# Performance work log

Hardware: AMD Instinct MI355X
Metric: run time of the kernel (lower is better)

Reference implementation:

```python
import jax, jax.numpy as jnp
import numpy as np

# pywt db8 reconstruction low-pass filter (rec_lo); other filters derived per pywt conventions
_REC_LO = np.array([
    0.05441584224308161, 0.3128715909144659, 0.6756307362980128,
    0.5853546836548691, -0.015829105256023893, -0.2840155429624281,
    0.00047248457399797254, 0.128747426620186, -0.01736930100202211,
    -0.04408825393106472, 0.013981027917015516, 0.008746094047015655,
    -0.00487035299301066, -0.0003917403729959771, 0.0006754494059985568,
    -0.00011747678400228192], dtype=np.float64)
_F = 16
_REC_HI = np.array([(-1.0) ** k * _REC_LO[_F - 1 - k] for k in range(_F)])  # qmf
_DEC_LO = _REC_LO[::-1].copy()
_DEC_HI = _REC_HI[::-1].copy()
# lax.conv does cross-correlation; np.convolve flips the filter, so pre-flip here
_DEC_K = np.ascontiguousarray(np.stack([_DEC_LO[::-1], _DEC_HI[::-1]])[:, None, :])  # [2,1,F]
_REC_K = np.ascontiguousarray(np.stack([_REC_LO[::-1], _REC_HI[::-1]])[None, :, :])  # [1,2,F]
_THRESHOLD_FACTOR = 1.0


def _dwt_last(x):
    # single-level DWT along last axis, pywt 'symmetric' boundary mode
    shp = x.shape
    xf = x.reshape(-1, 1, shp[-1])
    xe = jnp.pad(xf, ((0, 0), (0, 0), (_F - 1, _F - 1)), mode='symmetric')[:, :, 1:]
    y = jax.lax.conv_general_dilated(xe, jnp.asarray(_DEC_K, x.dtype), (2,), 'VALID',
                                     dimension_numbers=('NCW', 'OIW', 'NCW'))  # [M,2,n]
    n = y.shape[-1]  # n = floor((N + F - 1) / 2)
    return y[:, 0].reshape(shp[:-1] + (n,)), y[:, 1].reshape(shp[:-1] + (n,))


def _idwt_last(ca, cd, out_len):
    # single-level inverse DWT along last axis; out_len = 2*n - F + 2
    shp = ca.shape
    n = shp[-1]
    m = int(np.prod(shp[:-1]))
    u = jnp.zeros((m, 2, 2 * n), ca.dtype)
    u = u.at[:, 0, ::2].set(ca.reshape(m, n)).at[:, 1, ::2].set(cd.reshape(m, n))
    ue = jnp.pad(u, ((0, 0), (0, 0), (_F - 1, _F - 1)))
    y = jax.lax.conv_general_dilated(ue, jnp.asarray(_REC_K, ca.dtype), (1,), 'VALID',
                                     dimension_numbers=('NCW', 'OIW', 'NCW'))[:, 0]
    return y[:, _F - 2:_F - 2 + out_len].reshape(shp[:-1] + (out_len,))


def _forward(x):
    B, H, W, C = x.shape
    M = B * C
    xm = jnp.transpose(x, (0, 3, 1, 2)).reshape(M, H, W)
    # level-1 wavedec2: rows (W axis) then columns (H axis)
    lo, hi = _dwt_last(xm)                               # [M,H,nW]
    ll, lh = _dwt_last(jnp.swapaxes(lo, -1, -2))         # [M,nW,nH]
    hl, hh = _dwt_last(jnp.swapaxes(hi, -1, -2))         # [M,nW,nH]
    # universal threshold from median abs of all detail subbands, per sample/channel
    det = jnp.concatenate([lh.reshape(M, -1), hl.reshape(M, -1), hh.reshape(M, -1)], axis=-1)
    sigma = jnp.median(jnp.abs(det), axis=-1) / 0.6745
    t = (sigma * jnp.sqrt(2.0 * jnp.log(float(H * W))) * _THRESHOLD_FACTOR)[:, None, None]
    soft = lambda c: jnp.sign(c) * jnp.maximum(jnp.abs(c) - t, 0.0)
    lh, hl, hh = soft(lh), soft(hl), soft(hh)
    # waverec2: inverse along H then along W
    nH = ll.shape[-1]
    Hr = 2 * nH - _F + 2
    rl = jnp.swapaxes(_idwt_last(ll, lh, Hr), -1, -2)    # [M,Hr,nW]
    rh = jnp.swapaxes(_idwt_last(hl, hh, Hr), -1, -2)    # [M,Hr,nW]
    nW = rl.shape[-1]
    y = _idwt_last(rl, rh, 2 * nW - _F + 2)              # [M,Hr,Wr]
    y = y[:, :H, :W].reshape(B, C, H, W)
    return jnp.transpose(y, (0, 2, 3, 1)).astype(x.dtype)


def setup_inputs() -> dict:
    key = jax.random.key(0)
    x = jax.random.normal(key, (32, 512, 512, 3), dtype=jnp.float32)
    return {"x": x}


def reference(x):
    return _forward(x)
```

## Files before the change

kernel.cpp:

```cpp
#include <hip/hip_runtime.h>
#include <math.h>

#define B_   32
#define H_   512
#define W_   512
#define C_   3
#define M_   96
#define NW_  263
#define NH_  263
#define DETPER 69169
#define DETTOT 207507
#define DETSTRIDE 207508
#define NVEC 51876
#define KRANK  103753u

__device__ __constant__ float RLO[16] = {
    0.05441584224308161f,  0.3128715909144659f,   0.6756307362980128f,
    0.5853546836548691f,  -0.015829105256023893f, -0.2840155429624281f,
    0.00047248457399797254f, 0.128747426620186f,  -0.01736930100202211f,
   -0.04408825393106472f,  0.013981027917015516f,  0.008746094047015655f,
   -0.00487035299301066f, -0.0003917403729959771f, 0.0006754494059985568f,
   -0.00011747678400228192f};
__device__ __constant__ float RHI[16] = {
   -0.00011747678400228192f, -0.0006754494059985568f, -0.0003917403729959771f,
    0.00487035299301066f,     0.008746094047015655f,  -0.013981027917015516f,
   -0.04408825393106472f,     0.01736930100202211f,    0.128747426620186f,
   -0.00047248457399797254f, -0.2840155429624281f,     0.015829105256023893f,
    0.5853546836548691f,     -0.6756307362980128f,     0.3128715909144659f,
   -0.05441584224308161f};

__device__ __forceinline__ int refl(int q, int N) {
    if (q < 0)  return -q - 1;
    if (q >= N) return 2 * N - 1 - q;
    return q;
}

__device__ __forceinline__ float softthr(float v, float thr) {
    float a = fabsf(v) - thr;
    return a > 0.f ? copysignf(a, v) : 0.f;
}

__global__ __launch_bounds__(256) void k_zero(unsigned* __restrict__ p, int n) {
    int i = blockIdx.x * 256 + threadIdx.x;
    if (i < n) p[i] = 0u;
}

__global__ __launch_bounds__(256) void k_fwd(const float* __restrict__ x,
                                             float* __restrict__ ll,
                                             float* __restrict__ det) {
    __shared__ float sX[46 * 144];
    __shared__ float sLO[46 * 64], sHI[46 * 64];
    const int m   = blockIdx.x;
    const int jw0 = blockIdx.y * 64;
    const int jh0 = blockIdx.z * 16;
    const int b = m / 3, c = m - 3 * (m / 3);
    const int tid = threadIdx.x;
    const int prow0 = 2 * jh0 - 14, pcol0 = 2 * jw0 - 14;
    for (int l = tid; l < 46 * 142; l += 256) {
        int rr = l / 142, cl = l - rr * 142;
        int h = refl(prow0 + rr, H_);
        int w = refl(pcol0 + cl, W_);
        sX[rr * 144 + cl] = x[((size_t)(b * H_ + h) * W_ + w) * C_ + c];
    }
    __syncthreads();
    for (int l = tid; l < 46 * 64; l += 256) {
        int rr = l >> 6, j = l & 63;
        const float* px = &sX[rr * 144 + 2 * j];
        float al = 0.f, ah = 0.f;
#pragma unroll
        for (int k = 0; k < 16; ++k) {
            al = fmaf(px[k], RLO[k], al);
            ah = fmaf(px[k], RHI[k], ah);
        }
        sLO[l] = al;
        sHI[l] = ah;
    }
    __syncthreads();
    const int tx = tid & 63, ty = tid >> 6;
    const int jw = jw0 + tx;
    if (jw >= NW_) return;
    float* llp = ll + (size_t)m * DETPER;
    float* dp  = det + (size_t)m * DETSTRIDE;
#pragma unroll
    for (int i = 0; i < 4; ++i) {
        int dy = ty + 4 * i;
        int jh = jh0 + dy;
        if (jh >= NH_) continue;
        int rbase = 2 * dy;
        float a0 = 0.f, a1 = 0.f, a2 = 0.f, a3 = 0.f;
#pragma unroll
        for (int k = 0; k < 16; ++k) {
            float vl = sLO[(rbase + k) * 64 + tx];
            float vh = sHI[(rbase + k) * 64 + tx];
            a0 = fmaf(vl, RLO[k], a0);
            a1 = fmaf(vl, RHI[k], a1);
            a2 = fmaf(vh, RLO[k], a2);
            a3 = fmaf(vh, RHI[k], a3);
        }
        size_t o = (size_t)jh * NW_ + jw;
        llp[o] = a0;
        dp[o] = a1;
        dp[DETPER + o] = a2;
        dp[2 * DETPER + o] = a3;
    }
}

__global__ __launch_bounds__(256) void k_hist1(const float* __restrict__ det,
                                               unsigned* __restrict__ hist) {
    __shared__ unsigned h[2048];
    const int tid = threadIdx.x, m = blockIdx.x;
    for (int i = tid; i < 2048; i += 256) h[i] = 0u;
    __syncthreads();
    const float* dp = det + (size_t)m * DETSTRIDE;
    const float4* dp4 = (const float4*)dp;
    const int stride = gridDim.y * 256;
    for (int v = blockIdx.y * 256 + tid; v < NVEC; v += stride) {
        float4 f = dp4[v];
        atomicAdd(&h[__float_as_uint(fabsf(f.x)) >> 21], 1u);
        atomicAdd(&h[__float_as_uint(fabsf(f.y)) >> 21], 1u);
        atomicAdd(&h[__float_as_uint(fabsf(f.z)) >> 21], 1u);
        atomicAdd(&h[__float_as_uint(fabsf(f.w)) >> 21], 1u);
    }
    if (blockIdx.y == 0 && tid < DETTOT - 4 * NVEC) {
        unsigned u = __float_as_uint(fabsf(dp[4 * NVEC + tid]));
        atomicAdd(&h[u >> 21], 1u);
    }
    __syncthreads();
    for (int i = tid; i < 2048; i += 256)
        if (h[i]) atomicAdd(&hist[m * 2048 + i], h[i]);
}

__global__ __launch_bounds__(256) void k_hist2(const float* __restrict__ det,
                                               const int* __restrict__ selBin1,
                                               unsigned* __restrict__ hist) {
    __shared__ unsigned h[2048];
    const int tid = threadIdx.x, m = blockIdx.x;
    const unsigned target = (unsigned)selBin1[m];
    for (int i = tid; i < 2048; i += 256) h[i] = 0u;
    __syncthreads();
    const float* dp = det + (size_t)m * DETSTRIDE;
    const float4* dp4 = (const float4*)dp;
    const int stride = gridDim.y * 256;
    for (int v = blockIdx.y * 256 + tid; v < NVEC; v += stride) {
        float4 f = dp4[v];
        unsigned a = __float_as_uint(fabsf(f.x));
        unsigned b = __float_as_uint(fabsf(f.y));
        unsigned c = __float_as_uint(fabsf(f.z));
        unsigned d = __float_as_uint(fabsf(f.w));
        if ((a >> 21) == target) atomicAdd(&h[(a >> 10) & 0x7FFu], 1u);
        if ((b >> 21) == target) atomicAdd(&h[(b >> 10) & 0x7FFu], 1u);
        if ((c >> 21) == target) atomicAdd(&h[(c >> 10) & 0x7FFu], 1u);
        if ((d >> 21) == target) atomicAdd(&h[(d >> 10) & 0x7FFu], 1u);
    }
    if (blockIdx.y == 0 && tid < DETTOT - 4 * NVEC) {
        unsigned u = __float_as_uint(fabsf(dp[4 * NVEC + tid]));
        if ((u >> 21) == target) atomicAdd(&h[(u >> 10) & 0x7FFu], 1u);
    }
    __syncthreads();
    for (int i = tid; i < 2048; i += 256)
        if (h[i]) atomicAdd(&hist[m * 2048 + i], h[i]);
}

__global__ __launch_bounds__(256) void k_hist3(const float* __restrict__ det,
                                               const int* __restrict__ selBin1,
                                               const int* __restrict__ selBin2,
                                               unsigned* __restrict__ hist) {
    __shared__ unsigned h[1024];
    const int tid = threadIdx.x, m = blockIdx.x;
    const unsigned target = ((unsigned)selBin1[m] << 11) | (unsigned)selBin2[m];
    for (int i = tid; i < 1024; i += 256) h[i] = 0u;
    __syncthreads();
    const float* dp = det + (size_t)m * DETSTRIDE;
    const float4* dp4 = (const float4*)dp;
    const int stride = gridDim.y * 256;
    for (int v = blockIdx.y * 256 + tid; v < NVEC; v += stride) {
        float4 f = dp4[v];
        unsigned a = __float_as_uint(fabsf(f.x));
        unsigned b = __float_as_uint(fabsf(f.y));
        unsigned c = __float_as_uint(fabsf(f.z));
        unsigned d = __float_as_uint(fabsf(f.w));
        if ((a >> 10) == target) atomicAdd(&h[a & 0x3FFu], 1u);
        if ((b >> 10) == target) atomicAdd(&h[b & 0x3FFu], 1u);
        if ((c >> 10) == target) atomicAdd(&h[c & 0x3FFu], 1u);
        if ((d >> 10) == target) atomicAdd(&h[d & 0x3FFu], 1u);
    }
    if (blockIdx.y == 0 && tid < DETTOT - 4 * NVEC) {
        unsigned u = __float_as_uint(fabsf(dp[4 * NVEC + tid]));
        if ((u >> 10) == target) atomicAdd(&h[u & 0x3FFu], 1u);
    }
    __syncthreads();
    for (int i = tid; i < 1024; i += 256)
        if (h[i]) atomicAdd(&hist[m * 1024 + i], h[i]);
}

__device__ int histSelect(unsigned* hist, int nb, unsigned rank, unsigned* rem) {
    __shared__ unsigned ps[256];
    __shared__ int s_bin;
    __shared__ unsigned s_rem;
    const int tid = threadIdx.x;
    if (tid == 0) { s_bin = 0; s_rem = 0; }
    const int per = nb >> 8;
    unsigned s = 0;
    for (int i = 0; i < per; ++i) s += hist[tid * per + i];
    ps[tid] = s;
    __syncthreads();
    for (int off = 1; off < 256; off <<= 1) {
        unsigned v = ps[tid];
        unsigned add = (tid >= off) ? ps[tid - off] : 0u;
        __syncthreads();
        ps[tid] = v + add;
        __syncthreads();
    }
    unsigned incl = ps[tid], excl = incl - s;
    if (rank >= excl && rank < incl) {
        unsigned cum = excl;
        for (int i = 0; i < per; ++i) {
            unsigned c = hist[tid * per + i];
            if (cum + c > rank) { s_bin = tid * per + i; s_rem = rank - cum; break; }
            cum += c;
        }
    }
    __syncthreads();
    int rbin = s_bin;
    unsigned rr = s_rem;
    __syncthreads();
    *rem = rr;
    return rbin;
}

__global__ __launch_bounds__(256) void k_sel2048(const unsigned* __restrict__ hist,
                                                 const unsigned* __restrict__ rankIn,
                                                 int* __restrict__ selBin,
                                                 unsigned* __restrict__ rankOut) {
    __shared__ unsigned h[2048];
    const int m = blockIdx.x, tid = threadIdx.x;
    for (int i = tid; i < 2048; i += 256) h[i] = hist[m * 2048 + i];
    __syncthreads();
    unsigned rank = rankIn ? rankIn[m] : KRANK;
    unsigned rem;
    int bin = histSelect(h, 2048, rank, &rem);
    if (tid == 0) { selBin[m] = bin; rankOut[m] = rem; }
}

__global__ __launch_bounds__(256) void k_sel3(const unsigned* __restrict__ hist,
                                              const unsigned* __restrict__ rankIn,
                                              const int* __restrict__ selBin1,
                                              const int* __restrict__ selBin2,
                                              float* __restrict__ tval) {
    __shared__ unsigned h[1024];
    const int m = blockIdx.x, tid = threadIdx.x;
    for (int i = tid; i < 1024; i += 256) h[i] = hist[m * 1024 + i];
    __syncthreads();
    unsigned rem;
    int low = histSelect(h, 1024, rankIn[m], &rem);
    if (tid == 0) {
        unsigned bits = ((unsigned)selBin1[m] << 21) | ((unsigned)selBin2[m] << 10) | (unsigned)low;
        double med = (double)__uint_as_float(bits);
        tval[m] = (float)(med / 0.6745 * 4.995327667046959);
    }
}

__global__ __launch_bounds__(256) void k_inv(const float* __restrict__ ll,
                                             const float* __restrict__ det,
                                             const float* __restrict__ tval,
                                             float* __restrict__ out) {
    __shared__ float sLL[23 * 40], sLH[23 * 40], sHL[23 * 40], sHH[23 * 40];
    __shared__ float sRL[32 * 40], sRH[32 * 40];
    const int m  = blockIdx.x;
    const int w0 = blockIdx.y * 64;
    const int t0 = blockIdx.z * 32;
    const int b = m / 3, c = m - 3 * (m / 3);
    const int tid = threadIdx.x;
    const float thr = tval[m];
    const int jW0 = w0 >> 1, s0 = t0 >> 1;
    const float* llp = ll + (size_t)m * DETPER;
    const float* dp  = det + (size_t)m * DETSTRIDE;
    for (int l = tid; l < 23 * 39; l += 256) {
        int rr = l / 39, cc = l - rr * 39;
        size_t o = (size_t)(s0 + rr) * NW_ + (jW0 + cc);
        int li = rr * 40 + cc;
        sLL[li] = llp[o];
        sLH[li] = softthr(dp[o], thr);
        sHL[li] = softthr(dp[DETPER + o], thr);
        sHH[li] = softthr(dp[2 * DETPER + o], thr);
    }
    __syncthreads();
    for (int l = tid; l < 32 * 39; l += 256) {
        int tr = l / 39, cc = l - tr * 39;
        int srow = tr >> 1, r = tr & 1;
        float aL = 0.f, aH = 0.f;
#pragma unroll
        for (int a = 0; a < 8; ++a) {
            int li = (srow + 7 - a) * 40 + cc;
            float wl = RLO[2 * a + r], wh = RHI[2 * a + r];
            aL = fmaf(sLL[li], wl, fmaf(sLH[li], wh, aL));
            aH = fmaf(sHL[li], wl, fmaf(sHH[li], wh, aH));
        }
        sRL[tr * 40 + cc] = aL;
        sRH[tr * 40 + cc] = aH;
    }
    __syncthreads();
    for (int l = tid; l < 32 * 64; l += 256) {
        int tr = l >> 6, wloc = l & 63;
        int r = wloc & 1, jb = (wloc >> 1) + 7;
        float acc = 0.f;
#pragma unroll
        for (int a = 0; a < 8; ++a) {
            int li = tr * 40 + jb - a;
            acc = fmaf(sRL[li], RLO[2 * a + r], fmaf(sRH[li], RHI[2 * a + r], acc));
        }
        out[((size_t)(b * H_ + (t0 + tr)) * W_ + (w0 + wloc)) * C_ + c] = acc;
    }
}

extern "C" void kernel_launch(void* const* d_in, const int* in_sizes, int n_in,
                              void* d_out, int out_size, void* d_ws, size_t ws_size,
                              hipStream_t stream) {
    const float* x = (const float*)d_in[0];
    float* out = (float*)d_out;

    char* ws = (char*)d_ws;
    float* ll  = (float*)ws; ws += (size_t)M_ * DETPER * 4;
    float* det = (float*)ws; ws += (size_t)M_ * DETSTRIDE * 4;
    unsigned* hist1 = (unsigned*)ws; ws += (size_t)M_ * 2048 * 4;
    unsigned* hist2 = (unsigned*)ws; ws += (size_t)M_ * 2048 * 4;
    unsigned* hist3 = (unsigned*)ws; ws += (size_t)M_ * 1024 * 4;
    int*      selBin1 = (int*)ws;      ws += M_ * 4;
    int*      selBin2 = (int*)ws;      ws += M_ * 4;
    unsigned* rank1   = (unsigned*)ws; ws += M_ * 4;
    unsigned* rank2   = (unsigned*)ws; ws += M_ * 4;
    float*    tval    = (float*)ws;    ws += M_ * 4;

    const int histWords = M_ * (2048 + 2048 + 1024);
    k_zero   <<<dim3((histWords + 255) / 256), 256, 0, stream>>>(hist1, histWords);
    k_fwd    <<<dim3(M_, 5, 17),  256, 0, stream>>>(x, ll, det);
    k_hist1  <<<dim3(M_, 16),     256, 0, stream>>>(det, hist1);
    k_sel2048<<<dim3(M_),         256, 0, stream>>>(hist1, nullptr, selBin1, rank1);
    k_hist2  <<<dim3(M_, 16),     256, 0, stream>>>(det, selBin1, hist2);
    k_sel2048<<<dim3(M_),         256, 0, stream>>>(hist2, rank1, selBin2, rank2);
    k_hist3  <<<dim3(M_, 16),     256, 0, stream>>>(det, selBin1, selBin2, hist3);
    k_sel3   <<<dim3(M_),         256, 0, stream>>>(hist3, rank2, selBin1, selBin2, tval);
    k_inv    <<<dim3(M_, 8, 16),  256, 0, stream>>>(ll, det, tval, out);
}
```

Before: 432.6 us.

## Register-block forward and inverse DWT passes to reuse shared-memory loads

The forward kernel's row filter now computes four outputs per thread from one float4-loaded window, with padded shared strides. The column filter caches a 22-row strip in registers and produces four consecutive outputs per thread. The inverse kernel does the same for both passes: nine-row register windows feed four vertical outputs, and float4-loaded rows feed eight horizontal outputs per thread. The aim is fewer LDS reads per FMA, at the cost of more registers and possibly lower occupancy.

```diff
diff --git a/kernel.cpp b/kernel.cpp
--- a/kernel.cpp
+++ b/kernel.cpp
@@ -13,6 +13,9 @@
 #define DETSTRIDE 207508
 #define NVEC 51876
 #define KRANK  103753u
+
+#define SXS 148
+#define SLS 68
 
 __device__ __constant__ float RLO[16] = {
     0.05441584224308161f,  0.3128715909144659f,   0.6756307362980128f,
@@ -48,8 +51,8 @@
 __global__ __launch_bounds__(256) void k_fwd(const float* __restrict__ x,
                                              float* __restrict__ ll,
                                              float* __restrict__ det) {
-    __shared__ float sX[46 * 144];
-    __shared__ float sLO[46 * 64], sHI[46 * 64];
+    __shared__ float sX[46 * SXS];
+    __shared__ float sLO[46 * SLS], sHI[46 * SLS];
     const int m   = blockIdx.x;
     const int jw0 = blockIdx.y * 64;
     const int jh0 = blockIdx.z * 16;
@@ -60,42 +63,59 @@
         int rr = l / 142, cl = l - rr * 142;
         int h = refl(prow0 + rr, H_);
         int w = refl(pcol0 + cl, W_);
-        sX[rr * 144 + cl] = x[((size_t)(b * H_ + h) * W_ + w) * C_ + c];
-    }
-    __syncthreads();
-    for (int l = tid; l < 46 * 64; l += 256) {
-        int rr = l >> 6, j = l & 63;
-        const float* px = &sX[rr * 144 + 2 * j];
-        float al = 0.f, ah = 0.f;
-#pragma unroll
-        for (int k = 0; k < 16; ++k) {
-            al = fmaf(px[k], RLO[k], al);
-            ah = fmaf(px[k], RHI[k], ah);
-        }
-        sLO[l] = al;
-        sHI[l] = ah;
-    }
-    __syncthreads();
-    const int tx = tid & 63, ty = tid >> 6;
+        sX[rr * SXS + cl] = x[((size_t)(b * H_ + h) * W_ + w) * C_ + c];
+    }
+    __syncthreads();
+    {
+        const int q = (tid >> 2) & 15;
+        const int rbase = (tid & 3) + 4 * (tid >> 6);
+        auto rowdwt = [&](int rr) {
+            const float4* p4 = (const float4*)&sX[rr * SXS + 8 * q];
+            float4 f0 = p4[0], f1 = p4[1], f2 = p4[2], f3 = p4[3], f4v = p4[4], f5 = p4[5];
+            float v[24] = {f0.x,f0.y,f0.z,f0.w, f1.x,f1.y,f1.z,f1.w,
+                           f2.x,f2.y,f2.z,f2.w, f3.x,f3.y,f3.z,f3.w,
+                           f4v.x,f4v.y,f4v.z,f4v.w, f5.x,f5.y,f5.z,f5.w};
+            float lo0=0.f,lo1=0.f,lo2=0.f,lo3=0.f, hi0=0.f,hi1=0.f,hi2=0.f,hi3=0.f;
+#pragma unroll
+            for (int k = 0; k < 16; ++k) {
+                float w0 = RLO[k], w1 = RHI[k];
+                lo0 = fmaf(v[k],     w0, lo0);  hi0 = fmaf(v[k],     w1, hi0);
+                lo1 = fmaf(v[k + 2], w0, lo1);  hi1 = fmaf(v[k + 2], w1, hi1);
+                lo2 = fmaf(v[k + 4], w0, lo2);  hi2 = fmaf(v[k + 4], w1, hi2);
+                lo3 = fmaf(v[k + 6], w0, lo3);  hi3 = fmaf(v[k + 6], w1, hi3);
+            }
+            *(float4*)&sLO[rr * SLS + 4 * q] = make_float4(lo0, lo1, lo2, lo3);
+            *(float4*)&sHI[rr * SLS + 4 * q] = make_float4(hi0, hi1, hi2, hi3);
+        };
+        rowdwt(rbase);
+        rowdwt(rbase + 16);
+        if (rbase + 32 < 46) rowdwt(rbase + 32);
+    }
+    __syncthreads();
+    const int tx = tid & 63, tg = tid >> 6;
     const int jw = jw0 + tx;
     if (jw >= NW_) return;
+    float vl[22], vh[22];
+#pragma unroll
+    for (int s = 0; s < 22; ++s) {
+        int row = 8 * tg + s;
+        vl[s] = sLO[row * SLS + tx];
+        vh[s] = sHI[row * SLS + tx];
+    }
     float* llp = ll + (size_t)m * DETPER;
     float* dp  = det + (size_t)m * DETSTRIDE;
 #pragma unroll
-    for (int i = 0; i < 4; ++i) {
-        int dy = ty + 4 * i;
-        int jh = jh0 + dy;
+    for (int d = 0; d < 4; ++d) {
+        int jh = jh0 + 4 * tg + d;
         if (jh >= NH_) continue;
-        int rbase = 2 * dy;
         float a0 = 0.f, a1 = 0.f, a2 = 0.f, a3 = 0.f;
 #pragma unroll
         for (int k = 0; k < 16; ++k) {
-            float vl = sLO[(rbase + k) * 64 + tx];
-            float vh = sHI[(rbase + k) * 64 + tx];
-            a0 = fmaf(vl, RLO[k], a0);
-            a1 = fmaf(vl, RHI[k], a1);
-            a2 = fmaf(vh, RLO[k], a2);
-            a3 = fmaf(vh, RHI[k], a3);
+            float fl = vl[2 * d + k], fh = vh[2 * d + k];
+            a0 = fmaf(fl, RLO[k], a0);
+            a1 = fmaf(fl, RHI[k], a1);
+            a2 = fmaf(fh, RLO[k], a2);
+            a3 = fmaf(fh, RHI[k], a3);
         }
         size_t o = (size_t)jh * NW_ + jw;
         llp[o] = a0;
@@ -285,31 +305,52 @@
         sHH[li] = softthr(dp[2 * DETPER + o], thr);
     }
     __syncthreads();
-    for (int l = tid; l < 32 * 39; l += 256) {
-        int tr = l / 39, cc = l - tr * 39;
-        int srow = tr >> 1, r = tr & 1;
-        float aL = 0.f, aH = 0.f;
-#pragma unroll
-        for (int a = 0; a < 8; ++a) {
-            int li = (srow + 7 - a) * 40 + cc;
-            float wl = RLO[2 * a + r], wh = RHI[2 * a + r];
-            aL = fmaf(sLL[li], wl, fmaf(sLH[li], wh, aL));
-            aH = fmaf(sHL[li], wl, fmaf(sHH[li], wh, aH));
-        }
-        sRL[tr * 40 + cc] = aL;
-        sRH[tr * 40 + cc] = aH;
-    }
-    __syncthreads();
-    for (int l = tid; l < 32 * 64; l += 256) {
-        int tr = l >> 6, wloc = l & 63;
-        int r = wloc & 1, jb = (wloc >> 1) + 7;
-        float acc = 0.f;
-#pragma unroll
-        for (int a = 0; a < 8; ++a) {
-            int li = tr * 40 + jb - a;
-            acc = fmaf(sRL[li], RLO[2 * a + r], fmaf(sRH[li], RHI[2 * a + r], acc));
-        }
-        out[((size_t)(b * H_ + (t0 + tr)) * W_ + (w0 + wloc)) * C_ + c] = acc;
+    for (int l = tid; l < 8 * 39; l += 256) {
+        int tg = l / 39, cc = l - tg * 39;
+        float l9[9], d9[9], g9[9], h9[9];
+#pragma unroll
+        for (int s = 0; s < 9; ++s) {
+            int li = (2 * tg + s) * 40 + cc;
+            l9[s] = sLL[li]; d9[s] = sLH[li]; g9[s] = sHL[li]; h9[s] = sHH[li];
+        }
+#pragma unroll
+        for (int d = 0; d < 4; ++d) {
+            int sl = d >> 1, r = d & 1;
+            float aL = 0.f, aH = 0.f;
+#pragma unroll
+            for (int a = 0; a < 8; ++a) {
+                int s = sl + 7 - a;
+                float wl = RLO[2 * a + r], wh = RHI[2 * a + r];
+                aL = fmaf(l9[s], wl, fmaf(d9[s], wh, aL));
+                aH = fmaf(g9[s], wl, fmaf(h9[s], wh, aH));
+            }
+            sRL[(4 * tg + d) * 40 + cc] = aL;
+            sRH[(4 * tg + d) * 40 + cc] = aH;
+        }
+    }
+    __syncthreads();
+    {
+        const int tr = tid >> 3, jg = tid & 7;
+        const float4* pl = (const float4*)&sRL[tr * 40 + 4 * jg];
+        const float4* ph = (const float4*)&sRH[tr * 40 + 4 * jg];
+        float4 L0 = pl[0], L1 = pl[1], L2 = pl[2];
+        float4 K0 = ph[0], K1 = ph[1], K2 = ph[2];
+        float rl[12] = {L0.x,L0.y,L0.z,L0.w, L1.x,L1.y,L1.z,L1.w, L2.x,L2.y,L2.z,L2.w};
+        float rh[12] = {K0.x,K0.y,K0.z,K0.w, K1.x,K1.y,K1.z,K1.w, K2.x,K2.y,K2.z,K2.w};
+        size_t obase = ((size_t)(b * H_ + (t0 + tr)) * W_ + (w0 + 8 * jg)) * C_ + c;
+#pragma unroll
+        for (int u = 0; u < 4; ++u) {
+#pragma unroll
+            for (int r = 0; r < 2; ++r) {
+                float acc = 0.f;
+#pragma unroll
+                for (int a = 0; a < 8; ++a) {
+                    int s = u + 7 - a;
+                    acc = fmaf(rl[s], RLO[2 * a + r], fmaf(rh[s], RHI[2 * a + r], acc));
+                }
+                out[obase + (size_t)(2 * u + r) * C_] = acc;
+            }
+        }
     }
 }
 
```

Result: slower. 475.9 us (+10.0%).

## Stream input rows in chunks and register-cache column filter taps in forward DWT

Applied to the files above, without the earlier changes.

The forward DWT kernel now loads the input tile in 12-row chunks, running the row filter per chunk, which shrinks the sX shared buffer from 46 to 12 rows and cuts LDS footprint so more blocks can be resident. The column pass gives each thread 4 consecutive output rows and loads the 22 needed sLO/sHI values into registers once, instead of re-reading shared memory for every tap. The cost is extra __syncthreads per chunk and higher register pressure from the 44-float arrays.

```diff
diff --git a/kernel.cpp b/kernel.cpp
--- a/kernel.cpp
+++ b/kernel.cpp
@@ -13,6 +13,9 @@
 #define DETSTRIDE 207508
 #define NVEC 51876
 #define KRANK  103753u
+
+#define SXS 144
+#define CR  12
 
 __device__ __constant__ float RLO[16] = {
     0.05441584224308161f,  0.3128715909144659f,   0.6756307362980128f,
@@ -48,7 +51,7 @@
 __global__ __launch_bounds__(256) void k_fwd(const float* __restrict__ x,
                                              float* __restrict__ ll,
                                              float* __restrict__ det) {
-    __shared__ float sX[46 * 144];
+    __shared__ float sX[CR * SXS];
     __shared__ float sLO[46 * 64], sHI[46 * 64];
     const int m   = blockIdx.x;
     const int jw0 = blockIdx.y * 64;
@@ -56,46 +59,53 @@
     const int b = m / 3, c = m - 3 * (m / 3);
     const int tid = threadIdx.x;
     const int prow0 = 2 * jh0 - 14, pcol0 = 2 * jw0 - 14;
-    for (int l = tid; l < 46 * 142; l += 256) {
-        int rr = l / 142, cl = l - rr * 142;
-        int h = refl(prow0 + rr, H_);
-        int w = refl(pcol0 + cl, W_);
-        sX[rr * 144 + cl] = x[((size_t)(b * H_ + h) * W_ + w) * C_ + c];
-    }
-    __syncthreads();
-    for (int l = tid; l < 46 * 64; l += 256) {
-        int rr = l >> 6, j = l & 63;
-        const float* px = &sX[rr * 144 + 2 * j];
-        float al = 0.f, ah = 0.f;
-#pragma unroll
-        for (int k = 0; k < 16; ++k) {
-            al = fmaf(px[k], RLO[k], al);
-            ah = fmaf(px[k], RHI[k], ah);
-        }
-        sLO[l] = al;
-        sHI[l] = ah;
-    }
-    __syncthreads();
-    const int tx = tid & 63, ty = tid >> 6;
+    for (int r0 = 0; r0 < 46; r0 += CR) {
+        const int nr = (46 - r0) < CR ? (46 - r0) : CR;
+        for (int l = tid; l < nr * 142; l += 256) {
+            int rr = l / 142, cl = l - rr * 142;
+            int h = refl(prow0 + r0 + rr, H_);
+            int w = refl(pcol0 + cl, W_);
+            sX[rr * SXS + cl] = x[((size_t)(b * H_ + h) * W_ + w) * C_ + c];
+        }
+        __syncthreads();
+        for (int l = tid; l < nr * 64; l += 256) {
+            int rr = l >> 6, j = l & 63;
+            const float* px = &sX[rr * SXS + 2 * j];
+            float al = 0.f, ah = 0.f;
+#pragma unroll
+            for (int k = 0; k < 16; ++k) {
+                al = fmaf(px[k], RLO[k], al);
+                ah = fmaf(px[k], RHI[k], ah);
+            }
+            sLO[(r0 + rr) * 64 + j] = al;
+            sHI[(r0 + rr) * 64 + j] = ah;
+        }
+        __syncthreads();
+    }
+    const int tx = tid & 63, tg = tid >> 6;
     const int jw = jw0 + tx;
     if (jw >= NW_) return;
+    float vl[22], vh[22];
+#pragma unroll
+    for (int s = 0; s < 22; ++s) {
+        int row = 8 * tg + s;
+        vl[s] = sLO[row * 64 + tx];
+        vh[s] = sHI[row * 64 + tx];
+    }
     float* llp = ll + (size_t)m * DETPER;
     float* dp  = det + (size_t)m * DETSTRIDE;
 #pragma unroll
-    for (int i = 0; i < 4; ++i) {
-        int dy = ty + 4 * i;
-        int jh = jh0 + dy;
+    for (int d = 0; d < 4; ++d) {
+        int jh = jh0 + 4 * tg + d;
         if (jh >= NH_) continue;
-        int rbase = 2 * dy;
         float a0 = 0.f, a1 = 0.f, a2 = 0.f, a3 = 0.f;
 #pragma unroll
         for (int k = 0; k < 16; ++k) {
-            float vl = sLO[(rbase + k) * 64 + tx];
-            float vh = sHI[(rbase + k) * 64 + tx];
-            a0 = fmaf(vl, RLO[k], a0);
-            a1 = fmaf(vl, RHI[k], a1);
-            a2 = fmaf(vh, RLO[k], a2);
-            a3 = fmaf(vh, RHI[k], a3);
+            float fl = vl[2 * d + k], fh = vh[2 * d + k];
+            a0 = fmaf(fl, RLO[k], a0);
+            a1 = fmaf(fl, RHI[k], a1);
+            a2 = fmaf(fh, RLO[k], a2);
+            a3 = fmaf(fh, RHI[k], a3);
         }
         size_t o = (size_t)jh * NW_ + jw;
         llp[o] = a0;
```

New measurement: 435.7 us. Within noise of the previous version (+0.7%).
